# Kernel tuning notes

Measured on AMD Instinct MI355X. Metric: run time of the kernel, lower is better.

## Reference

```python
import jax, jax.numpy as jnp
import numpy as np

# dims matching init_kwargs / input_specs
N, C, H, W = 8, 256, 64, 64
OUT_C, KH, KW = 256, 3, 3
STRIDE, PAD = 1, 1
OUT_H = (H - KH + 2 * PAD) // STRIDE + 1  # 64
OUT_W = (W - KW + 2 * PAD) // STRIDE + 1  # 64
K = KH * KW


def setup_inputs() -> dict:
    key = jax.random.key(0)
    k1, k2, k3 = jax.random.split(key, 3)
    x = jax.random.normal(k1, (N, C, H, W), dtype=jnp.float32)
    offset = jax.random.normal(k2, (N, 2 * K, OUT_H, OUT_W), dtype=jnp.float32)
    # kaiming-uniform-ish scale for weight (fan_in = C*KH*KW)
    bound = 1.0 / np.sqrt(C * KH * KW)
    weight = jax.random.uniform(k3, (OUT_C, C, KH, KW), dtype=jnp.float32,
                                minval=-bound, maxval=bound)
    return {"input": x, "offset": offset, "weight": weight}


def _deform_conv(x, offset, weight):
    # base sampling positions in pixel coords: y = oy*stride + ky - pad
    ky = jnp.repeat(jnp.arange(KH, dtype=jnp.float32) - PAD, KW)  # [K]
    kx = jnp.tile(jnp.arange(KW, dtype=jnp.float32) - PAD, KH)    # [K]
    oy = jnp.arange(OUT_H, dtype=jnp.float32) * STRIDE            # [outH]
    ox = jnp.arange(OUT_W, dtype=jnp.float32) * STRIDE            # [outW]
    base_y = ky[:, None, None] + oy[None, :, None]  # [K, outH, 1]
    base_x = kx[:, None, None] + ox[None, None, :]  # [K, 1, outW]

    off = offset.reshape(N, K, 2, OUT_H, OUT_W)
    y = base_y[None] + off[:, :, 0]  # [N, K, outH, outW], offset channel 0 = dy
    xp = base_x[None] + off[:, :, 1]  # channel 1 = dx

    # bilinear sample with zero padding (grid_sample align_corners=True, zeros)
    y0 = jnp.floor(y)
    x0 = jnp.floor(xp)
    bidx = jnp.arange(N)[:, None, None, None]
    acc = jnp.zeros((N, K, OUT_H, OUT_W, C), dtype=x.dtype)
    for dy in (0.0, 1.0):
        for dx in (0.0, 1.0):
            yi = y0 + dy
            xi = x0 + dx
            wgt = (1.0 - jnp.abs(y - yi)) * (1.0 - jnp.abs(xp - xi))
            valid = ((yi >= 0) & (yi <= H - 1) & (xi >= 0) & (xi <= W - 1))
            yc = jnp.clip(yi, 0, H - 1).astype(jnp.int32)
            xc = jnp.clip(xi, 0, W - 1).astype(jnp.int32)
            g = x[bidx, :, yc, xc]  # [N, K, outH, outW, C]
            acc = acc + g * (wgt * valid.astype(x.dtype))[..., None]

    # weight.view(outC, -1) flattens (C, KH, KW) -> (C, K) ordering
    w = weight.reshape(OUT_C, C, K)
    out = jnp.einsum('nkhwc,ock->nohw', acc, w)  # [N, outC, outH, outW]
    return out


def reference(input, offset, weight):
    # NOTE: original forward never adds bias -> faithfully omitted
    return _deform_conv(input, offset, weight)
```

## Files before the change

### kernel.cpp

```cpp
#include <hip/hip_runtime.h>
#include <hip/hip_bf16.h>
#include <stdint.h>


typedef short short8 __attribute__((ext_vector_type(8)));
typedef float f32x4 __attribute__((ext_vector_type(4)));

__device__ __forceinline__ float bflo(uint32_t u) { return __uint_as_float(u << 16); }
__device__ __forceinline__ float bfhi(uint32_t u) { return __uint_as_float(u & 0xffff0000u); }
__device__ __forceinline__ uint32_t packbf(float a, float b) {
  unsigned short ua = __builtin_bit_cast(unsigned short, __float2bfloat16(a));
  unsigned short ub = __builtin_bit_cast(unsigned short, __float2bfloat16(b));
  return (uint32_t)ua | ((uint32_t)ub << 16);
}

__global__ __launch_bounds__(256) void prep_x_kernel(const float* __restrict__ x,
                                                     unsigned short* __restrict__ xb) {
  __shared__ float tile[64][65];
  int bn   = blockIdx.x >> 8;
  int rem  = blockIdx.x & 255;
  int y    = rem >> 2;
  int cblk = rem & 3;
  int tid  = threadIdx.x;
  const float* src = x + ((size_t)(bn * 256 + cblk * 64)) * 4096 + y * 64;
#pragma unroll
  for (int i = 0; i < 4; ++i) {
    int u  = i * 256 + tid;
    int cl = u >> 4;
    int xs = (u & 15) * 4;
    float4 v = *(const float4*)(src + cl * 4096 + xs);
    tile[cl][xs] = v.x; tile[cl][xs + 1] = v.y;
    tile[cl][xs + 2] = v.z; tile[cl][xs + 3] = v.w;
  }
  __syncthreads();
  unsigned short* dst = xb + ((size_t)(bn * 64 + y) * 64) * 256 + cblk * 64;
#pragma unroll
  for (int i = 0; i < 8; ++i) {
    int v2  = i * 256 + tid;
    int xc  = v2 >> 5;
    int cl2 = (v2 & 31) * 2;
    *(uint32_t*)(dst + xc * 256 + cl2) = packbf(tile[cl2][xc], tile[cl2 + 1][xc]);
  }
}

__global__ __launch_bounds__(256) void prep_w_kernel(const float* __restrict__ w,
                                                     unsigned short* __restrict__ w3s) {
  int idx = blockIdx.x * 256 + threadIdx.x;
  int t   = idx >> 14;
  int r2  = idx & 16383;
  int g   = r2 >> 3;
  int e   = r2 & 7;
  int oc  = g >> 3;
  int kk8 = (g & 7) ^ (oc & 7);
  int kk  = kk8 * 8 + e;
  int c   = (t & 3) * 64 + kk;
  int k   = t >> 2;
  w3s[idx] = __builtin_bit_cast(unsigned short, __float2bfloat16(w[(oc * 256 + c) * 9 + k]));
}

__device__ __forceinline__ void compute_coords(int bn, int oh, int k, int r,
                                               const float* __restrict__ offset,
                                               float4* cwp, int4* cpp) {
  int ky = k / 3 - 1;
  int kx = k % 3 - 1;
  float offy = offset[((bn * 18 + 2 * k    ) * 64 + oh) * 64 + r];
  float offx = offset[((bn * 18 + 2 * k + 1) * 64 + oh) * 64 + r];
  float y = (float)(oh + ky) + offy;
  float x = (float)(r + kx) + offx;
  float y0f = floorf(y), x0f = floorf(x);
  float fy = y - y0f, fx = x - x0f;
  int y0 = (int)y0f, x0 = (int)x0f;
  int y1 = y0 + 1, x1 = x0 + 1;
  float vy0 = (y0 >= 0 && y0 <= 63) ? 1.0f : 0.0f;
  float vy1 = (y1 >= 0 && y1 <= 63) ? 1.0f : 0.0f;
  float vx0 = (x0 >= 0 && x0 <= 63) ? 1.0f : 0.0f;
  float vx1 = (x1 >= 0 && x1 <= 63) ? 1.0f : 0.0f;
  float wy0 = (1.0f - fy) * vy0, wy1 = fy * vy1;
  float wx0 = (1.0f - fx) * vx0, wx1 = fx * vx1;
  *cwp = make_float4(wy0 * wx0, wy0 * wx1, wy1 * wx0, wy1 * wx1);
  int y0c = min(max(y0, 0), 63), y1c = min(max(y1, 0), 63);
  int x0c = min(max(x0, 0), 63), x1c = min(max(x1, 0), 63);
  *cpp = make_int4((y0c * 64 + x0c) * 512, (y0c * 64 + x1c) * 512,
                   (y1c * 64 + x0c) * 512, (y1c * 64 + x1c) * 512);
}

__global__ __launch_bounds__(512, 4) void deform_mfma_kernel(
    const unsigned short* __restrict__ xb,
    const float* __restrict__ offset,
    const unsigned short* __restrict__ w3s,
    float* __restrict__ out) {
  __shared__ __align__(16) unsigned short At[2][64 * 72];
  __shared__ __align__(16) unsigned short Bt[256 * 64];
  __shared__ float4 cw[2][64];
  __shared__ int4   cp[2][64];

  int bn  = blockIdx.x & 7;
  int oh  = blockIdx.x >> 3;
  int tid = threadIdx.x;

  int w     = tid >> 6;
  int lane  = tid & 63;
  int wrow  = w & 1;
  int wcol  = w >> 1;
  int half  = lane >> 5;
  int cpair = (lane & 31) * 2;
  int mrow  = lane & 15;
  int quad  = lane >> 4;

  if (tid < 128) {
    int k0 = tid >> 6, r = tid & 63;
    compute_coords(bn, oh, k0, r, offset, &cw[k0][r], &cp[k0][r]);
  }
  __syncthreads();

  f32x4 acc[2][4] = {};
  const unsigned short* xbn = xb + (size_t)bn * (64 * 64 * 256);

#define BDMA(TT)                                                                \
  {                                                                             \
    const unsigned short* src = w3s + (TT) * 16384;                             \
    _Pragma("unroll")                                                           \
    for (int j = 0; j < 4; ++j) {                                               \
      int base16 = j * 512 + w * 64;                                            \
      __builtin_amdgcn_global_load_lds(                                         \
          (const __attribute__((address_space(1))) void*)(src + (base16 + lane) * 8), \
          (__attribute__((address_space(3))) void*)(Bt + base16 * 8),           \
          16, 0, 0);                                                            \
    }                                                                           \
  }

#define ASTAGE(TT)                                                              \
  {                                                                             \
    int sel_ = ((TT) >> 2) & 1;                                                 \
    unsigned short* dst_ = At[(TT) & 1];                                        \
    const char* gb_ = (const char*)(xbn + ((TT) & 3) * 64 + cpair);             \
    _Pragma("unroll")                                                           \
    for (int j = 0; j < 4; ++j) {                                               \
      int r_ = w * 8 + j * 2 + half;                                            \
      float4 wv_ = cw[sel_][r_];                                                \
      int4   pv_ = cp[sel_][r_];                                                \
      uint32_t u00 = *(const uint32_t*)(gb_ + pv_.x);                           \
      uint32_t u01 = *(const uint32_t*)(gb_ + pv_.y);                           \
      uint32_t u10 = *(const uint32_t*)(gb_ + pv_.z);                           \
      uint32_t u11 = *(const uint32_t*)(gb_ + pv_.w);                           \
      float a0 = bflo(u00) * wv_.x + bflo(u01) * wv_.y + bflo(u10) * wv_.z + bflo(u11) * wv_.w; \
      float a1 = bfhi(u00) * wv_.x + bfhi(u01) * wv_.y + bfhi(u10) * wv_.z + bfhi(u11) * wv_.w; \
      *(uint32_t*)(&dst_[r_ * 72 + cpair]) = packbf(a0, a1);                    \
    }                                                                           \
  }

  BDMA(0)
  ASTAGE(0)
  __syncthreads();

  short8 bfr[2][4];

  for (int t = 0; t < 36; ++t) {
    int cur = t & 1;

#pragma unroll
    for (int ks = 0; ks < 2; ++ks)
#pragma unroll
      for (int nn = 0; nn < 4; ++nn) {
        int oc  = wcol * 64 + nn * 16 + mrow;
        int g16 = oc * 8 + ((ks * 4 + quad) ^ (mrow & 7));
        bfr[ks][nn] = *(const short8*)(Bt + g16 * 8);
      }
    __syncthreads();

    if (t < 35) {
      int s = t + 1;
      BDMA(s)
      ASTAGE(s)
      if ((s & 3) == 0 && s < 32 && tid < 64)
        compute_coords(bn, oh, (s >> 2) + 1, tid, offset,
                       &cw[((s >> 2) + 1) & 1][tid], &cp[((s >> 2) + 1) & 1][tid]);
    }

#pragma unroll
    for (int ks = 0; ks < 2; ++ks) {
      short8 af[2];
#pragma unroll
      for (int m = 0; m < 2; ++m)
        af[m] = *(const short8*)(&At[cur][(wrow * 32 + m * 16 + mrow) * 72 + ks * 32 + quad * 8]);
#pragma unroll
      for (int m = 0; m < 2; ++m)
#pragma unroll
        for (int nn = 0; nn < 4; ++nn)
          acc[m][nn] = __builtin_amdgcn_mfma_f32_16x16x32_bf16(af[m], bfr[ks][nn], acc[m][nn], 0, 0, 0);
    }
    __syncthreads();
  }

  float* outp = out + (size_t)(bn * 256) * 4096 + oh * 64;
#pragma unroll
  for (int m = 0; m < 2; ++m) {
    int ow0 = wrow * 32 + m * 16 + quad * 4;
#pragma unroll
    for (int nn = 0; nn < 4; ++nn) {
      int oc = wcol * 64 + nn * 16 + mrow;
      *(f32x4*)(outp + oc * 4096 + ow0) = acc[m][nn];
    }
  }
#undef BDMA
#undef ASTAGE
}

extern "C" void kernel_launch(void* const* d_in, const int* in_sizes, int n_in,
                              void* d_out, int out_size, void* d_ws, size_t ws_size,
                              hipStream_t stream) {
  (void)in_sizes; (void)n_in; (void)out_size; (void)ws_size;
  const float* x      = (const float*)d_in[0];
  const float* offset = (const float*)d_in[1];
  const float* weight = (const float*)d_in[2];
  float* out = (float*)d_out;

  unsigned short* xb  = (unsigned short*)d_ws;
  unsigned short* w3s = (unsigned short*)((char*)d_ws + (size_t)8*64*64*256*2);

  prep_x_kernel<<<2048, 256, 0, stream>>>(x, xb);
  prep_w_kernel<<<2304, 256, 0, stream>>>(weight, w3s);
  deform_mfma_kernel<<<512, 512, 0, stream>>>(xb, offset, w3s, out);
}
```

Before: 161.0 us.

## Precompute bilinear coords in prep kernel and vectorize A-tile gather to 16B

Bilinear weights and pixel indices are now computed for all positions in a fused weight/coord prep kernel and stored packed as fp16 weights plus 16-bit indices. The main kernel reads them per stage from global memory instead of computing them in shared memory. Each thread gathers 16-byte chunks (8 channels) per corner, replacing 4-byte loads, and the A tile drops its double buffer because A fragments are loaded into registers before the barrier. This cuts per-block coordinate work and gather instruction count, at the cost of an extra global coords buffer, fp16 rounding of the weights, and less LDS buffering.

```diff
diff --git a/kernel.cpp b/kernel.cpp
--- a/kernel.cpp
+++ b/kernel.cpp
@@ -1,5 +1,6 @@
 #include <hip/hip_runtime.h>
 #include <hip/hip_bf16.h>
+#include <hip/hip_fp16.h>
 #include <stdint.h>
 
 
@@ -12,6 +13,10 @@
   unsigned short ua = __builtin_bit_cast(unsigned short, __float2bfloat16(a));
   unsigned short ub = __builtin_bit_cast(unsigned short, __float2bfloat16(b));
   return (uint32_t)ua | ((uint32_t)ub << 16);
+}
+__device__ __forceinline__ float h2f(uint32_t bits16) {
+  __half h = __builtin_bit_cast(__half, (unsigned short)bits16);
+  return __half2float(h);
 }
 
 __global__ __launch_bounds__(256) void prep_x_kernel(const float* __restrict__ x,
@@ -43,56 +48,67 @@
   }
 }
 
-__global__ __launch_bounds__(256) void prep_w_kernel(const float* __restrict__ w,
-                                                     unsigned short* __restrict__ w3s) {
-  int idx = blockIdx.x * 256 + threadIdx.x;
-  int t   = idx >> 14;
-  int r2  = idx & 16383;
-  int g   = r2 >> 3;
-  int e   = r2 & 7;
-  int oc  = g >> 3;
-  int kk8 = (g & 7) ^ (oc & 7);
-  int kk  = kk8 * 8 + e;
-  int c   = (t & 3) * 64 + kk;
-  int k   = t >> 2;
-  w3s[idx] = __builtin_bit_cast(unsigned short, __float2bfloat16(w[(oc * 256 + c) * 9 + k]));
-}
-
-__device__ __forceinline__ void compute_coords(int bn, int oh, int k, int r,
-                                               const float* __restrict__ offset,
-                                               float4* cwp, int4* cpp) {
-  int ky = k / 3 - 1;
-  int kx = k % 3 - 1;
-  float offy = offset[((bn * 18 + 2 * k    ) * 64 + oh) * 64 + r];
-  float offx = offset[((bn * 18 + 2 * k + 1) * 64 + oh) * 64 + r];
-  float y = (float)(oh + ky) + offy;
-  float x = (float)(r + kx) + offx;
-  float y0f = floorf(y), x0f = floorf(x);
-  float fy = y - y0f, fx = x - x0f;
-  int y0 = (int)y0f, x0 = (int)x0f;
-  int y1 = y0 + 1, x1 = x0 + 1;
-  float vy0 = (y0 >= 0 && y0 <= 63) ? 1.0f : 0.0f;
-  float vy1 = (y1 >= 0 && y1 <= 63) ? 1.0f : 0.0f;
-  float vx0 = (x0 >= 0 && x0 <= 63) ? 1.0f : 0.0f;
-  float vx1 = (x1 >= 0 && x1 <= 63) ? 1.0f : 0.0f;
-  float wy0 = (1.0f - fy) * vy0, wy1 = fy * vy1;
-  float wx0 = (1.0f - fx) * vx0, wx1 = fx * vx1;
-  *cwp = make_float4(wy0 * wx0, wy0 * wx1, wy1 * wx0, wy1 * wx1);
-  int y0c = min(max(y0, 0), 63), y1c = min(max(y1, 0), 63);
-  int x0c = min(max(x0, 0), 63), x1c = min(max(x1, 0), 63);
-  *cpp = make_int4((y0c * 64 + x0c) * 512, (y0c * 64 + x1c) * 512,
-                   (y1c * 64 + x0c) * 512, (y1c * 64 + x1c) * 512);
+__global__ __launch_bounds__(256) void prep_wc_kernel(const float* __restrict__ w,
+                                                      const float* __restrict__ offset,
+                                                      unsigned short* __restrict__ w3s,
+                                                      unsigned short* __restrict__ coords) {
+  if (blockIdx.x < 2304) {
+    int idx = blockIdx.x * 256 + threadIdx.x;
+    int t   = idx >> 14;
+    int r2  = idx & 16383;
+    int g   = r2 >> 3;
+    int e   = r2 & 7;
+    int oc  = g >> 3;
+    int kk8 = (g & 7) ^ (oc & 7);
+    int kk  = kk8 * 8 + e;
+    int c   = (t & 3) * 64 + kk;
+    int k   = t >> 2;
+    w3s[idx] = __builtin_bit_cast(unsigned short, __float2bfloat16(w[(oc * 256 + c) * 9 + k]));
+  } else {
+    int idx = (blockIdx.x - 2304) * 256 + threadIdx.x;
+    int ow  = idx & 63;
+    int oh  = (idx >> 6) & 63;
+    int r   = idx >> 12;
+    int k   = r % 9;
+    int bn  = r / 9;
+    int ky = k / 3 - 1;
+    int kx = k % 3 - 1;
+    float offy = offset[((bn * 18 + 2 * k    ) * 64 + oh) * 64 + ow];
+    float offx = offset[((bn * 18 + 2 * k + 1) * 64 + oh) * 64 + ow];
+    float y = (float)(oh + ky) + offy;
+    float x = (float)(ow + kx) + offx;
+    float y0f = floorf(y), x0f = floorf(x);
+    float fy = y - y0f, fx = x - x0f;
+    int y0 = (int)y0f, x0 = (int)x0f;
+    int y1 = y0 + 1, x1 = x0 + 1;
+    float vy0 = (y0 >= 0 && y0 <= 63) ? 1.0f : 0.0f;
+    float vy1 = (y1 >= 0 && y1 <= 63) ? 1.0f : 0.0f;
+    float vx0 = (x0 >= 0 && x0 <= 63) ? 1.0f : 0.0f;
+    float vx1 = (x1 >= 0 && x1 <= 63) ? 1.0f : 0.0f;
+    float wy0 = (1.0f - fy) * vy0, wy1 = fy * vy1;
+    float wx0 = (1.0f - fx) * vx0, wx1 = fx * vx1;
+    int y0c = min(max(y0, 0), 63), y1c = min(max(y1, 0), 63);
+    int x0c = min(max(x0, 0), 63), x1c = min(max(x1, 0), 63);
+    unsigned short ent[8];
+    ent[0] = __builtin_bit_cast(unsigned short, __float2half(wy0 * wx0));
+    ent[1] = __builtin_bit_cast(unsigned short, __float2half(wy0 * wx1));
+    ent[2] = __builtin_bit_cast(unsigned short, __float2half(wy1 * wx0));
+    ent[3] = __builtin_bit_cast(unsigned short, __float2half(wy1 * wx1));
+    ent[4] = (unsigned short)(y0c * 64 + x0c);
+    ent[5] = (unsigned short)(y0c * 64 + x1c);
+    ent[6] = (unsigned short)(y1c * 64 + x0c);
+    ent[7] = (unsigned short)(y1c * 64 + x1c);
+    *(uint4*)(coords + (size_t)idx * 8) = *(const uint4*)ent;
+  }
 }
 
 __global__ __launch_bounds__(512, 4) void deform_mfma_kernel(
     const unsigned short* __restrict__ xb,
-    const float* __restrict__ offset,
+    const unsigned short* __restrict__ coords,
     const unsigned short* __restrict__ w3s,
     float* __restrict__ out) {
-  __shared__ __align__(16) unsigned short At[2][64 * 72];
+  __shared__ __align__(16) unsigned short At[64 * 72];
   __shared__ __align__(16) unsigned short Bt[256 * 64];
-  __shared__ float4 cw[2][64];
-  __shared__ int4   cp[2][64];
 
   int bn  = blockIdx.x & 7;
   int oh  = blockIdx.x >> 3;
@@ -102,19 +118,17 @@
   int lane  = tid & 63;
   int wrow  = w & 1;
   int wcol  = w >> 1;
-  int half  = lane >> 5;
-  int cpair = (lane & 31) * 2;
   int mrow  = lane & 15;
   int quad  = lane >> 4;
 
-  if (tid < 128) {
-    int k0 = tid >> 6, r = tid & 63;
-    compute_coords(bn, oh, k0, r, offset, &cw[k0][r], &cp[k0][r]);
-  }
-  __syncthreads();
+  int srow = tid >> 3;
+  int sg   = tid & 7;
+
+  const unsigned short* xbn = xb + (size_t)bn * (64 * 64 * 256);
+  const char* gbase = (const char*)xbn + sg * 16;
+  const unsigned short* cbase = coords + ((size_t)((bn * 9) * 64 + oh) * 64 + srow) * 8;
 
   f32x4 acc[2][4] = {};
-  const unsigned short* xbn = xb + (size_t)bn * (64 * 64 * 256);
 
 #define BDMA(TT)                                                                \
   {                                                                             \
@@ -131,64 +145,61 @@
 
 #define ASTAGE(TT)                                                              \
   {                                                                             \
-    int sel_ = ((TT) >> 2) & 1;                                                 \
-    unsigned short* dst_ = At[(TT) & 1];                                        \
-    const char* gb_ = (const char*)(xbn + ((TT) & 3) * 64 + cpair);             \
-    _Pragma("unroll")                                                           \
-    for (int j = 0; j < 4; ++j) {                                               \
-      int r_ = w * 8 + j * 2 + half;                                            \
-      float4 wv_ = cw[sel_][r_];                                                \
-      int4   pv_ = cp[sel_][r_];                                                \
-      uint32_t u00 = *(const uint32_t*)(gb_ + pv_.x);                           \
-      uint32_t u01 = *(const uint32_t*)(gb_ + pv_.y);                           \
-      uint32_t u10 = *(const uint32_t*)(gb_ + pv_.z);                           \
-      uint32_t u11 = *(const uint32_t*)(gb_ + pv_.w);                           \
-      float a0 = bflo(u00) * wv_.x + bflo(u01) * wv_.y + bflo(u10) * wv_.z + bflo(u11) * wv_.w; \
-      float a1 = bfhi(u00) * wv_.x + bfhi(u01) * wv_.y + bfhi(u10) * wv_.z + bfhi(u11) * wv_.w; \
-      *(uint32_t*)(&dst_[r_ * 72 + cpair]) = packbf(a0, a1);                    \
-    }                                                                           \
+    uint4 e = *(const uint4*)(cbase + ((TT) >> 2) * 32768);                     \
+    const char* gb = gbase + ((TT) & 3) * 128;                                  \
+    uint4 c00 = *(const uint4*)(gb + ((e.z & 0xffffu) << 9));                   \
+    uint4 c01 = *(const uint4*)(gb + ((e.z >> 16) << 9));                       \
+    uint4 c10 = *(const uint4*)(gb + ((e.w & 0xffffu) << 9));                   \
+    uint4 c11 = *(const uint4*)(gb + ((e.w >> 16) << 9));                       \
+    float w00 = h2f(e.x & 0xffffu), w01 = h2f(e.x >> 16);                       \
+    float w10 = h2f(e.y & 0xffffu), w11 = h2f(e.y >> 16);                       \
+    float a0 = bflo(c00.x) * w00 + bflo(c01.x) * w01 + bflo(c10.x) * w10 + bflo(c11.x) * w11; \
+    float a1 = bfhi(c00.x) * w00 + bfhi(c01.x) * w01 + bfhi(c10.x) * w10 + bfhi(c11.x) * w11; \
+    float a2 = bflo(c00.y) * w00 + bflo(c01.y) * w01 + bflo(c10.y) * w10 + bflo(c11.y) * w11; \
+    float a3 = bfhi(c00.y) * w00 + bfhi(c01.y) * w01 + bfhi(c10.y) * w10 + bfhi(c11.y) * w11; \
+    float a4 = bflo(c00.z) * w00 + bflo(c01.z) * w01 + bflo(c10.z) * w10 + bflo(c11.z) * w11; \
+    float a5 = bfhi(c00.z) * w00 + bfhi(c01.z) * w01 + bfhi(c10.z) * w10 + bfhi(c11.z) * w11; \
+    float a6 = bflo(c00.w) * w00 + bflo(c01.w) * w01 + bflo(c10.w) * w10 + bflo(c11.w) * w11; \
+    float a7 = bfhi(c00.w) * w00 + bfhi(c01.w) * w01 + bfhi(c10.w) * w10 + bfhi(c11.w) * w11; \
+    uint4 pk;                                                                   \
+    pk.x = packbf(a0, a1); pk.y = packbf(a2, a3);                               \
+    pk.z = packbf(a4, a5); pk.w = packbf(a6, a7);                               \
+    *(uint4*)(&At[srow * 72 + sg * 8]) = pk;                                    \
   }
 
   BDMA(0)
   ASTAGE(0)
   __syncthreads();
 
+  short8 af[2][2];
   short8 bfr[2][4];
 
   for (int t = 0; t < 36; ++t) {
-    int cur = t & 1;
-
-#pragma unroll
-    for (int ks = 0; ks < 2; ++ks)
+#pragma unroll
+    for (int ks = 0; ks < 2; ++ks) {
+#pragma unroll
+      for (int m = 0; m < 2; ++m)
+        af[m][ks] = *(const short8*)(&At[(wrow * 32 + m * 16 + mrow) * 72 + ks * 32 + quad * 8]);
 #pragma unroll
       for (int nn = 0; nn < 4; ++nn) {
         int oc  = wcol * 64 + nn * 16 + mrow;
         int g16 = oc * 8 + ((ks * 4 + quad) ^ (mrow & 7));
         bfr[ks][nn] = *(const short8*)(Bt + g16 * 8);
       }
+    }
     __syncthreads();
 
     if (t < 35) {
-      int s = t + 1;
-      BDMA(s)
-      ASTAGE(s)
-      if ((s & 3) == 0 && s < 32 && tid < 64)
-        compute_coords(bn, oh, (s >> 2) + 1, tid, offset,
-                       &cw[((s >> 2) + 1) & 1][tid], &cp[((s >> 2) + 1) & 1][tid]);
+      BDMA(t + 1)
+      ASTAGE(t + 1)
     }
-
-#pragma unroll
-    for (int ks = 0; ks < 2; ++ks) {
-      short8 af[2];
+#pragma unroll
+    for (int ks = 0; ks < 2; ++ks)
 #pragma unroll
       for (int m = 0; m < 2; ++m)
-        af[m] = *(const short8*)(&At[cur][(wrow * 32 + m * 16 + mrow) * 72 + ks * 32 + quad * 8]);
-#pragma unroll
-      for (int m = 0; m < 2; ++m)
 #pragma unroll
         for (int nn = 0; nn < 4; ++nn)
-          acc[m][nn] = __builtin_amdgcn_mfma_f32_16x16x32_bf16(af[m], bfr[ks][nn], acc[m][nn], 0, 0, 0);
-    }
+          acc[m][nn] = __builtin_amdgcn_mfma_f32_16x16x32_bf16(af[m][ks], bfr[ks][nn], acc[m][nn], 0, 0, 0);
     __syncthreads();
   }
 
@@ -215,10 +226,11 @@
   const float* weight = (const float*)d_in[2];
   float* out = (float*)d_out;
 
-  unsigned short* xb  = (unsigned short*)d_ws;
-  unsigned short* w3s = (unsigned short*)((char*)d_ws + (size_t)8*64*64*256*2);
+  unsigned short* xb     = (unsigned short*)d_ws;
+  unsigned short* w3s    = xb + (size_t)8 * 64 * 64 * 256;
+  unsigned short* coords = w3s + (size_t)36 * 16384;
 
   prep_x_kernel<<<2048, 256, 0, stream>>>(x, xb);
-  prep_w_kernel<<<2304, 256, 0, stream>>>(weight, w3s);
-  deform_mfma_kernel<<<512, 512, 0, stream>>>(xb, offset, w3s, out);
-}
+  prep_wc_kernel<<<3456, 256, 0, stream>>>(weight, offset, w3s, coords);
+  deform_mfma_kernel<<<512, 512, 0, stream>>>(xb, coords, w3s, out);
+}
```

After: 155.3 us. 3.6% less time.
